# Kernel optimization log

Hardware: AMD Instinct MI355X
Metric: run time of the kernel (lower is better)

Reference implementation:

```python
import jax, jax.numpy as jnp
import numpy as np

B, N, U = 16, 1024, 64  # batch, nodes, num_units
ALPHA = 0.2  # LeakyReLU negative slope
NEG = -9e15


def setup_inputs() -> dict:
    key = jax.random.key(0)
    ks = jax.random.split(key, 7)
    X = jax.random.normal(ks[0], (B, N, U), dtype=jnp.float32)
    state = jax.random.normal(ks[1], (B, N, U), dtype=jnp.float32)
    # random sparse adjacency (avg degree ~32) with self-loops
    adj = (jax.random.uniform(ks[2], (N, N)) < 32.0 / N).astype(jnp.float32)
    adj = jnp.maximum(adj, jnp.eye(N, dtype=jnp.float32))
    def xavier(k, shape):
        fan_in, fan_out = shape
        s = 1.414 * np.sqrt(6.0 / (fan_in + fan_out))
        return jax.random.uniform(k, shape, jnp.float32, -s, s)
    W1 = xavier(ks[3], (2 * U, 2 * U))   # gat_1: in 2U -> out 2U
    a1 = xavier(ks[4], (4 * U, 1))       # attention vector, 2*out
    W2 = xavier(ks[5], (2 * U, U))       # gat_2: in 2U -> out U
    a2 = xavier(ks[6], (2 * U, 1))
    return {"X": X, "state": state, "adj": adj, "W1": W1, "a1": a1, "W2": W2, "a2": a2}


def _gat_layer(x, adj, W, a):
    # x: [b,n,f_in], W: [f_in,F], a: [2F,1]
    h = jnp.einsum('bnf,fo->bno', x, W)              # [b,n,F]
    F_out = W.shape[1]
    s_src = h @ a[:F_out, 0]                         # [b,n] contribution of node i
    s_dst = h @ a[F_out:, 0]                         # [b,n] contribution of node j
    e = jax.nn.leaky_relu(s_src[:, :, None] + s_dst[:, None, :], ALPHA)  # [b,n,n]
    e = jnp.where(adj[None, :, :] > 0, e, NEG)
    att = jax.nn.softmax(e, axis=2)                  # masked softmax over neighbors j
    return jnp.einsum('bij,bjf->bif', att, h)        # [b,n,F]


def reference(X, state, adj, W1, a1, W2, a2):
    X1 = jnp.concatenate([X, state], axis=2)         # [b,n,2U]
    gv = jax.nn.sigmoid(_gat_layer(X1, adj, W1, a1)) # [b,n,2U]
    r, z = jnp.split(gv, 2, axis=2)                  # each [b,n,U]
    X2 = jnp.concatenate([X, r * state], axis=2)
    h_t1 = jnp.tanh(_gat_layer(X2, adj, W2, a2))     # [b,n,U]
    new_h = z * state + (1.0 - z) * h_t1
    return new_h
```

## Files before the change

kernel.cpp:

```cpp
#include <hip/hip_runtime.h>

#define BB 16
#define NN 1024
#define LALPHA 0.2f
#define MAXD 192

__global__ void build_csr(const float* __restrict__ adj, int* __restrict__ deg,
                          int* __restrict__ cols) {
    __shared__ int cnt;
    int i = blockIdx.x;
    if (threadIdx.x == 0) cnt = 0;
    __syncthreads();
    for (int j = threadIdx.x; j < NN; j += blockDim.x) {
        if (adj[(size_t)i * NN + j] > 0.0f) {
            int p = atomicAdd(&cnt, 1);
            if (p < MAXD) cols[(size_t)i * MAXD + p] = j;
        }
    }
    __syncthreads();
    if (threadIdx.x == 0) deg[i] = cnt < MAXD ? cnt : MAXD;
}

template <int FOUT, int RB>
__global__ void gemm_score(const float* __restrict__ A0, const float* __restrict__ A1,
                           const float* __restrict__ W, const float* __restrict__ avec,
                           float* __restrict__ h, float* __restrict__ s_src,
                           float* __restrict__ s_dst) {
    constexpr int TFN = FOUT / 4;
    constexpr int NT = (RB / 4) * TFN;
    __shared__ float xs[RB][132];
    int t = threadIdx.x;
    int tf = t % TFN, tr = t / TFN;
    int f0 = tf * 4, r0 = tr * 4;
    int base = blockIdx.x * RB;

    for (int idx = t; idx < RB * 32; idx += NT) {
        int r = idx >> 5, c = (idx & 31) * 4;
        float4 v = (c < 64) ? *(const float4*)(A0 + (size_t)(base + r) * 64 + c)
                            : *(const float4*)(A1 + (size_t)(base + r) * 64 + (c - 64));
        xs[r][c] = v.x; xs[r][c + 1] = v.y; xs[r][c + 2] = v.z; xs[r][c + 3] = v.w;
    }
    __syncthreads();

    float acc[4][4] = {};
    for (int k = 0; k < 128; k += 4) {
        float4 xv[4], wv[4];
#pragma unroll
        for (int i = 0; i < 4; i++) xv[i] = *(const float4*)&xs[r0 + i][k];
#pragma unroll
        for (int i = 0; i < 4; i++) wv[i] = *(const float4*)(W + (size_t)(k + i) * FOUT + f0);
#pragma unroll
        for (int i = 0; i < 4; i++) {
            float xr[4] = {xv[i].x, xv[i].y, xv[i].z, xv[i].w};
#pragma unroll
            for (int kk = 0; kk < 4; kk++) {
                acc[i][0] += xr[kk] * wv[kk].x;
                acc[i][1] += xr[kk] * wv[kk].y;
                acc[i][2] += xr[kk] * wv[kk].z;
                acc[i][3] += xr[kk] * wv[kk].w;
            }
        }
    }

    float a_s[4], a_d[4];
#pragma unroll
    for (int i = 0; i < 4; i++) {
        a_s[i] = avec[f0 + i];
        a_d[i] = avec[FOUT + f0 + i];
    }
#pragma unroll
    for (int i = 0; i < 4; i++) {
        int m = base + r0 + i;
        *(float4*)(h + (size_t)m * FOUT + f0) =
            make_float4(acc[i][0], acc[i][1], acc[i][2], acc[i][3]);
        float ps = acc[i][0] * a_s[0] + acc[i][1] * a_s[1] + acc[i][2] * a_s[2] + acc[i][3] * a_s[3];
        float pd = acc[i][0] * a_d[0] + acc[i][1] * a_d[1] + acc[i][2] * a_d[2] + acc[i][3] * a_d[3];
#pragma unroll
        for (int o = TFN / 2; o >= 1; o >>= 1) {
            ps += __shfl_xor(ps, o);
            pd += __shfl_xor(pd, o);
        }
        if (tf == 0) {
            s_src[m] = ps;
            s_dst[m] = pd;
        }
    }
}

__global__ __launch_bounds__(64) void attn1_kernel(
    const int* __restrict__ deg, const int* __restrict__ cols,
    const float* __restrict__ h1, const float* __restrict__ s_src,
    const float* __restrict__ s_dst, const float* __restrict__ state,
    float* __restrict__ rstate, float* __restrict__ zbuf) {
    int bi = blockIdx.x;
    int i = bi & (NN - 1);
    int b = bi >> 10;
    int lane = threadIdx.x;
    int d = deg[i];
    float ssrc = s_src[bi];
    __shared__ float w[MAXD + 4];
    __shared__ int cl[MAXD + 4];

    float ev[3];
    float mx = -1e30f;
    int s = 0;
    for (int j = lane; j < d; j += 64, s++) {
        int c = cols[(size_t)i * MAXD + j];
        cl[j] = c;
        float e = ssrc + s_dst[b * NN + c];
        e = e > 0.f ? e : LALPHA * e;
        ev[s] = e;
        mx = fmaxf(mx, e);
    }
#pragma unroll
    for (int o = 32; o >= 1; o >>= 1) mx = fmaxf(mx, __shfl_xor(mx, o));
    float sum = 0.f;
    s = 0;
    for (int j = lane; j < d; j += 64, s++) {
        float p = __expf(ev[s] - mx);
        w[j] = p;
        sum += p;
    }
#pragma unroll
    for (int o = 32; o >= 1; o >>= 1) sum += __shfl_xor(sum, o);
    if (lane < 4) {
        w[d + lane] = 0.f;
        cl[d + lane] = 0;
    }
    __syncthreads();
    float inv = 1.f / sum;

    const float* hb = h1 + (size_t)b * NN * 128 + lane * 2;
    int de4 = (d + 3) & ~3;
    float ax = 0.f, ay = 0.f;
    for (int j = 0; j < de4; j += 4) {
        float2 r0 = *(const float2*)(hb + (size_t)cl[j] * 128);
        float2 r1 = *(const float2*)(hb + (size_t)cl[j + 1] * 128);
        float2 r2 = *(const float2*)(hb + (size_t)cl[j + 2] * 128);
        float2 r3 = *(const float2*)(hb + (size_t)cl[j + 3] * 128);
        float w0 = w[j], w1 = w[j + 1], w2 = w[j + 2], w3 = w[j + 3];
        ax += w0 * r0.x + w1 * r1.x + w2 * r2.x + w3 * r3.x;
        ay += w0 * r0.y + w1 * r1.y + w2 * r2.y + w3 * r3.y;
    }
    float gx = 1.f / (1.f + __expf(-ax * inv));
    float gy = 1.f / (1.f + __expf(-ay * inv));
    if (lane < 32) {
        float2 st = *(const float2*)(state + (size_t)bi * 64 + lane * 2);
        *(float2*)(rstate + (size_t)bi * 64 + lane * 2) = make_float2(gx * st.x, gy * st.y);
    } else {
        int l2 = lane - 32;
        *(float2*)(zbuf + (size_t)bi * 64 + l2 * 2) = make_float2(gx, gy);
    }
}

__global__ __launch_bounds__(64) void attn2_kernel(
    const int* __restrict__ deg, const int* __restrict__ cols,
    const float* __restrict__ h2, const float* __restrict__ s_src,
    const float* __restrict__ s_dst, const float* __restrict__ state,
    const float* __restrict__ zbuf, float* __restrict__ out) {
    int bi = blockIdx.x;
    int i = bi & (NN - 1);
    int b = bi >> 10;
    int lane = threadIdx.x;
    int half = lane >> 5;
    int fl = lane & 31;
    int d = deg[i];
    float ssrc = s_src[bi];
    __shared__ float w[MAXD + 4];
    __shared__ int cl[MAXD + 4];

    float ev[3];
    float mx = -1e30f;
    int s = 0;
    for (int j = lane; j < d; j += 64, s++) {
        int c = cols[(size_t)i * MAXD + j];
        cl[j] = c;
        float e = ssrc + s_dst[b * NN + c];
        e = e > 0.f ? e : LALPHA * e;
        ev[s] = e;
        mx = fmaxf(mx, e);
    }
#pragma unroll
    for (int o = 32; o >= 1; o >>= 1) mx = fmaxf(mx, __shfl_xor(mx, o));
    float sum = 0.f;
    s = 0;
    for (int j = lane; j < d; j += 64, s++) {
        float p = __expf(ev[s] - mx);
        w[j] = p;
        sum += p;
    }
#pragma unroll
    for (int o = 32; o >= 1; o >>= 1) sum += __shfl_xor(sum, o);
    if (lane < 4) {
        w[d + lane] = 0.f;
        cl[d + lane] = 0;
    }
    __syncthreads();
    float inv = 1.f / sum;

    const float* hb = h2 + (size_t)b * NN * 64 + fl * 2;
    int de4 = (d + 3) & ~3;
    float ax = 0.f, ay = 0.f;
    for (int j = 0; j < de4; j += 4) {
        int i0 = j + half, i1 = j + 2 + half;
        float2 r0 = *(const float2*)(hb + (size_t)cl[i0] * 64);
        float2 r1 = *(const float2*)(hb + (size_t)cl[i1] * 64);
        float w0 = w[i0], w1 = w[i1];
        ax += w0 * r0.x + w1 * r1.x;
        ay += w0 * r0.y + w1 * r1.y;
    }
    ax += __shfl_xor(ax, 32);
    ay += __shfl_xor(ay, 32);
    if (lane < 32) {
        float hx = tanhf(ax * inv);
        float hy = tanhf(ay * inv);
        float2 z2 = *(const float2*)(zbuf + (size_t)bi * 64 + lane * 2);
        float2 st = *(const float2*)(state + (size_t)bi * 64 + lane * 2);
        *(float2*)(out + (size_t)bi * 64 + lane * 2) =
            make_float2(z2.x * st.x + (1.f - z2.x) * hx,
                        z2.y * st.y + (1.f - z2.y) * hy);
    }
}

extern "C" void kernel_launch(void* const* d_in, const int* in_sizes, int n_in,
                              void* d_out, int out_size, void* d_ws, size_t ws_size,
                              hipStream_t stream) {
    const float* X     = (const float*)d_in[0];
    const float* state = (const float*)d_in[1];
    const float* adj   = (const float*)d_in[2];
    const float* W1    = (const float*)d_in[3];
    const float* a1    = (const float*)d_in[4];
    const float* W2    = (const float*)d_in[5];
    const float* a2    = (const float*)d_in[6];
    float* out = (float*)d_out;

    char* ws = (char*)d_ws;
    size_t off = 0;
    auto alloc = [&](size_t bytes) -> void* {
        void* p = ws + off;
        off = (off + bytes + 255) & ~(size_t)255;
        return p;
    };
    int*   deg    = (int*)alloc(NN * sizeof(int));
    int*   cols   = (int*)alloc((size_t)NN * MAXD * sizeof(int));
    float* h1     = (float*)alloc((size_t)BB * NN * 128 * sizeof(float));
    float* ssrc1  = (float*)alloc((size_t)BB * NN * sizeof(float));
    float* sdst1  = (float*)alloc((size_t)BB * NN * sizeof(float));
    float* rstate = (float*)alloc((size_t)BB * NN * 64 * sizeof(float));
    float* zbuf   = (float*)alloc((size_t)BB * NN * 64 * sizeof(float));
    float* h2     = (float*)alloc((size_t)BB * NN * 64 * sizeof(float));
    float* ssrc2  = (float*)alloc((size_t)BB * NN * sizeof(float));
    float* sdst2  = (float*)alloc((size_t)BB * NN * sizeof(float));

    const int M = BB * NN;

    build_csr<<<NN, 256, 0, stream>>>(adj, deg, cols);
    gemm_score<128, 32><<<M / 32, 256, 0, stream>>>(X, state, W1, a1, h1, ssrc1, sdst1);
    attn1_kernel<<<M, 64, 0, stream>>>(deg, cols, h1, ssrc1, sdst1, state, rstate, zbuf);
    gemm_score<64, 64><<<M / 64, 256, 0, stream>>>(X, rstate, W2, a2, h2, ssrc2, sdst2);
    attn2_kernel<<<M, 64, 0, stream>>>(deg, cols, h2, ssrc2, sdst2, state, zbuf, out);
}
```

Before: 146.9 us.

## Swizzle block-to-batch mapping for XCD locality and pack four nodes per block

Block indices in both GEMM and attention kernels are remapped so consecutive blocks spread across batches in an interleaved pattern (blk&7, bit 3), which likely groups each batch's work onto one XCD so the gathered h rows stay in that die's L2. The attention kernels also move from one 64-thread block per node to 256-thread blocks holding four wavefronts, each handling a node with its own shared-memory slice. This cuts block launch overhead. The risk is that the __syncthreads now spans four waves, so a wave with a larger neighbor count can stall the others.

```diff
diff --git a/kernel.cpp b/kernel.cpp
--- a/kernel.cpp
+++ b/kernel.cpp
@@ -32,7 +32,10 @@
     int t = threadIdx.x;
     int tf = t % TFN, tr = t / TFN;
     int f0 = tf * 4, r0 = tr * 4;
-    int base = blockIdx.x * RB;
+    int blk = blockIdx.x;
+    int bb = (blk & 7) * 2 + ((blk >> 3) & 1);
+    int tile = blk >> 4;
+    int base = bb * NN + tile * RB;
 
     for (int idx = t; idx < RB * 32; idx += NT) {
         int r = idx >> 5, c = (idx & 31) * 4;
@@ -87,26 +90,28 @@
     }
 }
 
-__global__ __launch_bounds__(64) void attn1_kernel(
+__global__ __launch_bounds__(256) void attn1_kernel(
     const int* __restrict__ deg, const int* __restrict__ cols,
     const float* __restrict__ h1, const float* __restrict__ s_src,
     const float* __restrict__ s_dst, const float* __restrict__ state,
     float* __restrict__ rstate, float* __restrict__ zbuf) {
-    int bi = blockIdx.x;
-    int i = bi & (NN - 1);
-    int b = bi >> 10;
-    int lane = threadIdx.x;
+    int wv = threadIdx.x >> 6;
+    int lane = threadIdx.x & 63;
+    int blk = blockIdx.x;
+    int b = (blk & 7) * 2 + ((blk >> 3) & 1);
+    int i = (blk >> 4) * 4 + wv;
+    int bi = b * NN + i;
     int d = deg[i];
     float ssrc = s_src[bi];
-    __shared__ float w[MAXD + 4];
-    __shared__ int cl[MAXD + 4];
+    __shared__ float w[4][MAXD + 4];
+    __shared__ int cl[4][MAXD + 4];
 
     float ev[3];
     float mx = -1e30f;
     int s = 0;
     for (int j = lane; j < d; j += 64, s++) {
         int c = cols[(size_t)i * MAXD + j];
-        cl[j] = c;
+        cl[wv][j] = c;
         float e = ssrc + s_dst[b * NN + c];
         e = e > 0.f ? e : LALPHA * e;
         ev[s] = e;
@@ -118,14 +123,14 @@
     s = 0;
     for (int j = lane; j < d; j += 64, s++) {
         float p = __expf(ev[s] - mx);
-        w[j] = p;
+        w[wv][j] = p;
         sum += p;
     }
 #pragma unroll
     for (int o = 32; o >= 1; o >>= 1) sum += __shfl_xor(sum, o);
     if (lane < 4) {
-        w[d + lane] = 0.f;
-        cl[d + lane] = 0;
+        w[wv][d + lane] = 0.f;
+        cl[wv][d + lane] = 0;
     }
     __syncthreads();
     float inv = 1.f / sum;
@@ -134,11 +139,11 @@
     int de4 = (d + 3) & ~3;
     float ax = 0.f, ay = 0.f;
     for (int j = 0; j < de4; j += 4) {
-        float2 r0 = *(const float2*)(hb + (size_t)cl[j] * 128);
-        float2 r1 = *(const float2*)(hb + (size_t)cl[j + 1] * 128);
-        float2 r2 = *(const float2*)(hb + (size_t)cl[j + 2] * 128);
-        float2 r3 = *(const float2*)(hb + (size_t)cl[j + 3] * 128);
-        float w0 = w[j], w1 = w[j + 1], w2 = w[j + 2], w3 = w[j + 3];
+        float2 r0 = *(const float2*)(hb + (size_t)cl[wv][j] * 128);
+        float2 r1 = *(const float2*)(hb + (size_t)cl[wv][j + 1] * 128);
+        float2 r2 = *(const float2*)(hb + (size_t)cl[wv][j + 2] * 128);
+        float2 r3 = *(const float2*)(hb + (size_t)cl[wv][j + 3] * 128);
+        float w0 = w[wv][j], w1 = w[wv][j + 1], w2 = w[wv][j + 2], w3 = w[wv][j + 3];
         ax += w0 * r0.x + w1 * r1.x + w2 * r2.x + w3 * r3.x;
         ay += w0 * r0.y + w1 * r1.y + w2 * r2.y + w3 * r3.y;
     }
@@ -153,28 +158,30 @@
     }
 }
 
-__global__ __launch_bounds__(64) void attn2_kernel(
+__global__ __launch_bounds__(256) void attn2_kernel(
     const int* __restrict__ deg, const int* __restrict__ cols,
     const float* __restrict__ h2, const float* __restrict__ s_src,
     const float* __restrict__ s_dst, const float* __restrict__ state,
     const float* __restrict__ zbuf, float* __restrict__ out) {
-    int bi = blockIdx.x;
-    int i = bi & (NN - 1);
-    int b = bi >> 10;
-    int lane = threadIdx.x;
+    int wv = threadIdx.x >> 6;
+    int lane = threadIdx.x & 63;
+    int blk = blockIdx.x;
+    int b = (blk & 7) * 2 + ((blk >> 3) & 1);
+    int i = (blk >> 4) * 4 + wv;
+    int bi = b * NN + i;
     int half = lane >> 5;
     int fl = lane & 31;
     int d = deg[i];
     float ssrc = s_src[bi];
-    __shared__ float w[MAXD + 4];
-    __shared__ int cl[MAXD + 4];
+    __shared__ float w[4][MAXD + 4];
+    __shared__ int cl[4][MAXD + 4];
 
     float ev[3];
     float mx = -1e30f;
     int s = 0;
     for (int j = lane; j < d; j += 64, s++) {
         int c = cols[(size_t)i * MAXD + j];
-        cl[j] = c;
+        cl[wv][j] = c;
         float e = ssrc + s_dst[b * NN + c];
         e = e > 0.f ? e : LALPHA * e;
         ev[s] = e;
@@ -186,14 +193,14 @@
     s = 0;
     for (int j = lane; j < d; j += 64, s++) {
         float p = __expf(ev[s] - mx);
-        w[j] = p;
+        w[wv][j] = p;
         sum += p;
     }
 #pragma unroll
     for (int o = 32; o >= 1; o >>= 1) sum += __shfl_xor(sum, o);
     if (lane < 4) {
-        w[d + lane] = 0.f;
-        cl[d + lane] = 0;
+        w[wv][d + lane] = 0.f;
+        cl[wv][d + lane] = 0;
     }
     __syncthreads();
     float inv = 1.f / sum;
@@ -203,9 +210,9 @@
     float ax = 0.f, ay = 0.f;
     for (int j = 0; j < de4; j += 4) {
         int i0 = j + half, i1 = j + 2 + half;
-        float2 r0 = *(const float2*)(hb + (size_t)cl[i0] * 64);
-        float2 r1 = *(const float2*)(hb + (size_t)cl[i1] * 64);
-        float w0 = w[i0], w1 = w[i1];
+        float2 r0 = *(const float2*)(hb + (size_t)cl[wv][i0] * 64);
+        float2 r1 = *(const float2*)(hb + (size_t)cl[wv][i1] * 64);
+        float w0 = w[wv][i0], w1 = w[wv][i1];
         ax += w0 * r0.x + w1 * r1.x;
         ay += w0 * r0.y + w1 * r1.y;
     }
@@ -256,7 +263,7 @@
 
     build_csr<<<NN, 256, 0, stream>>>(adj, deg, cols);
     gemm_score<128, 32><<<M / 32, 256, 0, stream>>>(X, state, W1, a1, h1, ssrc1, sdst1);
-    attn1_kernel<<<M, 64, 0, stream>>>(deg, cols, h1, ssrc1, sdst1, state, rstate, zbuf);
+    attn1_kernel<<<M / 4, 256, 0, stream>>>(deg, cols, h1, ssrc1, sdst1, state, rstate, zbuf);
     gemm_score<64, 64><<<M / 64, 256, 0, stream>>>(X, rstate, W2, a2, h2, ssrc2, sdst2);
-    attn2_kernel<<<M, 64, 0, stream>>>(deg, cols, h2, ssrc2, sdst2, state, zbuf, out);
-}
+    attn2_kernel<<<M / 4, 256, 0, stream>>>(deg, cols, h2, ssrc2, sdst2, state, zbuf, out);
+}
```

Result: no change. 148.9 us (+1.4%).
